# Optimization experiments

Measured on AMD Instinct MI355X. Metric: run time of the kernel, lower is better.

## Reference

```python
import jax, jax.numpy as jnp
import numpy as np

V, E, H, L = 32000, 1024, 1024, 2
B, T = 64, 256


def setup_inputs() -> dict:
    key = jax.random.key(0)
    ks = jax.random.split(key, 6)
    src = jax.random.randint(ks[0], (B, T), 0, V, dtype=jnp.int32)
    s_e = 1.0 / np.sqrt(H)
    emb = jax.random.normal(ks[1], (V, E), dtype=jnp.float32) * 0.02
    # stacked-layer LSTM params; layer 0 input = E == H so shapes are uniform
    W_ih = jax.random.uniform(ks[2], (L, 4 * H, H), dtype=jnp.float32, minval=-s_e, maxval=s_e)
    W_hh = jax.random.uniform(ks[3], (L, 4 * H, H), dtype=jnp.float32, minval=-s_e, maxval=s_e)
    b_ih = jax.random.uniform(ks[4], (L, 4 * H), dtype=jnp.float32, minval=-s_e, maxval=s_e)
    b_hh = jax.random.uniform(ks[5], (L, 4 * H), dtype=jnp.float32, minval=-s_e, maxval=s_e)
    return {"src": src, "emb": emb, "W_ih": W_ih, "W_hh": W_hh, "b_ih": b_ih, "b_hh": b_hh}


def _lstm_stack(embedded, W_ih, W_hh, b_ih, b_hh):
    # embedded: [B, T, E]
    Bsz = embedded.shape[0]
    h0 = jnp.zeros((L, Bsz, H), embedded.dtype)
    c0 = jnp.zeros((L, Bsz, H), embedded.dtype)

    def step(carry, x_t):
        h, c = carry  # each [L, B, H]
        x = x_t       # [B, E]
        new_h, new_c = [], []
        for l in range(L):
            gates = x @ W_ih[l].T + b_ih[l] + h[l] @ W_hh[l].T + b_hh[l]  # [B, 4H]
            i, f, g, o = jnp.split(gates, 4, axis=-1)
            c_t = jax.nn.sigmoid(f) * c[l] + jax.nn.sigmoid(i) * jnp.tanh(g)
            h_t = jax.nn.sigmoid(o) * jnp.tanh(c_t)
            new_h.append(h_t)
            new_c.append(c_t)
            x = h_t  # feed to next layer (dropout p=0)
        return (jnp.stack(new_h), jnp.stack(new_c)), x

    (h_n, c_n), outs = jax.lax.scan(step, (h0, c0), jnp.swapaxes(embedded, 0, 1))
    return jnp.swapaxes(outs, 0, 1), h_n, c_n  # [B,T,H], [L,B,H], [L,B,H]


def reference(src, emb, W_ih, W_hh, b_ih, b_hh):
    embedded = emb[src]  # [B, T, E]
    encoder_outputs, h_n, c_n = _lstm_stack(embedded, W_ih, W_hh, b_ih, b_hh)
    return encoder_outputs, (h_n, c_n)
```

## Files before the change

kernel.cpp:

```cpp
#include <hip/hip_runtime.h>
#include <hip/hip_bf16.h>

typedef __hip_bfloat16 bf16;
typedef __attribute__((ext_vector_type(8))) short s16x8;
typedef __attribute__((ext_vector_type(4))) float f32x4;
typedef __attribute__((ext_vector_type(4))) int   i32x4;

#define BATCH   64
#define SEQ     256
#define HID     1024
#define GATES   4096
#define NWG     256
#define THREADS 256
#define UNITS   8
#define NCOLS   32
#define ROWSTRIDE 2056
#define BH      (BATCH * HID)

#define HBASE_OFF  4096ull
#define WS_NEED    (HBASE_OFF + 2ull * SEQ * BH * 2)
#define H0_RS 8
#define H1_RS 2

#define OUT_HN  ((size_t)BATCH * SEQ * HID)
#define OUT_CN  (OUT_HN + 2ull * BATCH * HID)

__device__ __forceinline__ short f2bf(float f) {
    unsigned int u = __builtin_bit_cast(unsigned int, f);
    u = (u + 0x7fffu + ((u >> 16) & 1u)) >> 16;
    return (short)u;
}

#define GLD(i, OFF, CF) asm volatile("global_load_dwordx4 %0, %1, off offset:" OFF " " CF \
                                     : "=v"(h[i]) : "v"(xrow));
#define MM8(B0) \
    _Pragma("unroll") \
    for (int kk = (B0); kk < (B0) + 8; ++kk) { \
        s16x8 b0 = *(const s16x8*)(s0 + kk * 32); \
        s16x8 b1 = *(const s16x8*)(s1 + kk * 32); \
        s16x8 av = __builtin_bit_cast(s16x8, h[kk]); \
        a0 = __builtin_amdgcn_mfma_f32_16x16x32_bf16(av, b0, a0, 0, 0, 0); \
        a1 = __builtin_amdgcn_mfma_f32_16x16x32_bf16(av, b1, a1, 0, 0, 0); \
    }
#define GEMM_FN(NAME, CF) \
__device__ __forceinline__ void NAME(const bf16* xrow, const bf16* s0, const bf16* s1, \
                                     f32x4& a0, f32x4& a1) \
{ \
    i32x4 h[32]; \
    GLD(0,"0",CF)    GLD(1,"64",CF)   GLD(2,"128",CF)  GLD(3,"192",CF) \
    GLD(4,"256",CF)  GLD(5,"320",CF)  GLD(6,"384",CF)  GLD(7,"448",CF) \
    GLD(8,"512",CF)  GLD(9,"576",CF)  GLD(10,"640",CF) GLD(11,"704",CF) \
    GLD(12,"768",CF) GLD(13,"832",CF) GLD(14,"896",CF) GLD(15,"960",CF) \
    GLD(16,"1024",CF) GLD(17,"1088",CF) GLD(18,"1152",CF) GLD(19,"1216",CF) \
    GLD(20,"1280",CF) GLD(21,"1344",CF) GLD(22,"1408",CF) GLD(23,"1472",CF) \
    asm volatile("s_waitcnt vmcnt(16)"); __builtin_amdgcn_sched_barrier(0); \
    MM8(0) \
    GLD(24,"1536",CF) GLD(25,"1600",CF) GLD(26,"1664",CF) GLD(27,"1728",CF) \
    GLD(28,"1792",CF) GLD(29,"1856",CF) GLD(30,"1920",CF) GLD(31,"1984",CF) \
    asm volatile("s_waitcnt vmcnt(16)"); __builtin_amdgcn_sched_barrier(0); \
    MM8(8) \
    asm volatile("s_waitcnt vmcnt(8)");  __builtin_amdgcn_sched_barrier(0); \
    MM8(16) \
    asm volatile("s_waitcnt vmcnt(0)");  __builtin_amdgcn_sched_barrier(0); \
    MM8(24) \
}
GEMM_FN(gemm_bt, "sc0 sc1")
GEMM_FN(gemm_p,  "")

__device__ __forceinline__ void gemm_f32c(const float* xrow, const bf16* s0, const bf16* s1,
                                          f32x4& a0, f32x4& a1)
{
#pragma unroll
    for (int c = 0; c < 4; ++c) {
        f32x4 xv[16];
#pragma unroll
        for (int i = 0; i < 8; ++i) {
            const float* p = xrow + (c * 8 + i) * 32;
            xv[2 * i]     = *(const f32x4*)p;
            xv[2 * i + 1] = *(const f32x4*)(p + 4);
        }
#pragma unroll
        for (int i = 0; i < 8; ++i) {
            const int kk = c * 8 + i;
            s16x8 af;
#pragma unroll
            for (int j = 0; j < 4; ++j) {
                af[j]     = f2bf(xv[2 * i][j]);
                af[4 + j] = f2bf(xv[2 * i + 1][j]);
            }
            s16x8 b0 = *(const s16x8*)(s0 + kk * 32);
            s16x8 b1 = *(const s16x8*)(s1 + kk * 32);
            a0 = __builtin_amdgcn_mfma_f32_16x16x32_bf16(af, b0, a0, 0, 0, 0);
            a1 = __builtin_amdgcn_mfma_f32_16x16x32_bf16(af, b1, a1, 0, 0, 0);
        }
    }
}

__device__ __forceinline__ void wave_poll(unsigned int* f, int tgt, int* seen) {
    if (tgt <= 0 || *seen >= tgt) return;
    const int l = threadIdx.x & 63;
    unsigned int* p0 = f + l;
    unsigned int* p1 = f + 64 + l;
    int a, b;
    for (;;) {
        a = (int)__hip_atomic_load(p0, __ATOMIC_RELAXED, __HIP_MEMORY_SCOPE_AGENT);
        b = (int)__hip_atomic_load(p1, __ATOMIC_RELAXED, __HIP_MEMORY_SCOPE_AGENT);
        if (__all((a >= tgt) && (b >= tgt))) break;
        __builtin_amdgcn_s_sleep(1);
    }
    int v = (a < b) ? a : b;
#pragma unroll
    for (int off = 32; off; off >>= 1) {
        int w = __shfl_xor(v, off, 64);
        v = (w < v) ? w : v;
    }
    *seen = v;
    asm volatile("" ::: "memory");
}

__global__ void ws_init(unsigned int* p, int n) {
    for (int i = blockIdx.x * blockDim.x + threadIdx.x; i < n; i += gridDim.x * blockDim.x)
        p[i] = 0u;
}

__global__ void __launch_bounds__(THREADS, 1)
lstm_enc(const int* __restrict__ src, const float* __restrict__ Wemb,
         const float* __restrict__ Wih, const float* __restrict__ Whh,
         const float* __restrict__ bih, const float* __restrict__ bhh,
         float* __restrict__ out, bf16* __restrict__ hbuf, int hist_on)
{
    __shared__ __align__(16) bf16 slab[NCOLS][ROWSTRIDE];
    __shared__ float bias[NCOLS];

    const int wg    = blockIdx.x;
    const int layer = wg >> 7;
    const int wgl   = wg & 127;
    const int j0    = wgl * UNITS;
    const int tid   = threadIdx.x;
    const int lane  = tid & 63;
    const int wave  = tid >> 6;
    const int m     = lane & 15;
    const int q     = lane >> 4;
    const int kq    = q * 8;
    const int b_a   = wave * 16 + m;

    for (int r = 0; r < NCOLS; ++r) {
        int g = r >> 3, u = r & 7;
        size_t grow = (size_t)layer * GATES * HID + (size_t)(g * HID + j0 + u) * HID;
        int k = tid * 8;
        const float* s = (k < HID) ? (Wih + grow + k) : (Whh + grow + (k - HID));
        s16x8 v;
#pragma unroll
        for (int j = 0; j < 8; ++j) v[j] = f2bf(s[j]);
        *(s16x8*)&slab[r][k] = v;
    }
    if (tid < NCOLS) {
        int g = tid >> 3, u = tid & 7;
        int off = layer * GATES + g * HID + j0 + u;
        bias[tid] = bih[off] + bhh[off];
    }
    __syncthreads();

    unsigned int* flags = (unsigned int*)hbuf;
    bf16* hb = (bf16*)((char*)hbuf + HBASE_OFF);
    bf16* h0 = hb;
    bf16* h1 = hist_on ? hb + (size_t)SEQ * BH : hb + (size_t)H0_RS * BH;
    unsigned int* f0 = flags + wave * 128;
    unsigned int* f1 = flags + 512 + wave * 128;
    unsigned int* myflag = flags + layer * 512 + wave * 128 + wgl;

    const int u = m & 7;
    const float b_i = bias[u], b_f = bias[8 + u], b_g = bias[16 + u], b_o = bias[24 + u];
    float c_s[4] = {0.f, 0.f, 0.f, 0.f};
    int seenA = 0, seenB = 0;

    int sv = (layer == 0) ? src[b_a * SEQ] : 0;

    for (int t = 0; t < SEQ; ++t) {
        f32x4 acc0 = {0.f, 0.f, 0.f, 0.f};
        f32x4 acc1 = {0.f, 0.f, 0.f, 0.f};

        if (layer == 0) {
            const float* xF = Wemb + (size_t)sv * HID + kq;
            if (t + 1 < SEQ) sv = src[b_a * SEQ + t + 1];
            gemm_f32c(xF, &slab[m][kq], &slab[16 + m][kq], acc0, acc1);
            wave_poll(f0, t, &seenA);
            if (t >= 1) {
                if (hist_on)
                    gemm_p(h0 + (size_t)(t - 1) * BH + b_a * HID + kq,
                           &slab[m][HID + kq], &slab[16 + m][HID + kq], acc0, acc1);
                else
                    gemm_bt(h0 + (size_t)((t - 1) & (H0_RS - 1)) * BH + b_a * HID + kq,
                            &slab[m][HID + kq], &slab[16 + m][HID + kq], acc0, acc1);
            }
            if (!hist_on)
                wave_poll(f1, t - 7, &seenB);
        } else {
            wave_poll(f0, t + 1, &seenA);
            if (hist_on)
                gemm_p(h0 + (size_t)t * BH + b_a * HID + kq,
                       &slab[m][kq], &slab[16 + m][kq], acc0, acc1);
            else
                gemm_bt(h0 + (size_t)(t & (H0_RS - 1)) * BH + b_a * HID + kq,
                        &slab[m][kq], &slab[16 + m][kq], acc0, acc1);
            wave_poll(f1, t, &seenB);
            if (t >= 1) {
                if (hist_on)
                    gemm_p(h1 + (size_t)(t - 1) * BH + b_a * HID + kq,
                           &slab[m][HID + kq], &slab[16 + m][HID + kq], acc0, acc1);
                else
                    gemm_bt(h1 + (size_t)((t - 1) & (H1_RS - 1)) * BH + b_a * HID + kq,
                            &slab[m][HID + kq], &slab[16 + m][HID + kq], acc0, acc1);
            }
        }

        float hval[4];
#pragma unroll
        for (int r = 0; r < 4; ++r) {
            float p0 = __shfl_xor(acc0[r], 8, 64);
            float p1 = __shfl_xor(acc1[r], 8, 64);
            const bool lo = (m < 8);
            float gi = (lo ? acc0[r] : p0) + b_i;
            float gf = (lo ? p0 : acc0[r]) + b_f;
            float gg = (lo ? acc1[r] : p1) + b_g;
            float go = (lo ? p1 : acc1[r]) + b_o;
            float si = 1.f / (1.f + __expf(-gi));
            float sf = 1.f / (1.f + __expf(-gf));
            float so = 1.f / (1.f + __expf(-go));
            c_s[r] = sf * c_s[r] + si * tanhf(gg);
            hval[r] = so * tanhf(c_s[r]);
        }

        bf16* hw = (layer == 0)
            ? h0 + (size_t)(hist_on ? t : (t & (H0_RS - 1))) * BH
            : h1 + (size_t)(hist_on ? t : (t & (H1_RS - 1))) * BH;
        if (m < 8) {
#pragma unroll
            for (int r = 0; r < 4; ++r) {
                int R = wave * 16 + q * 4 + r;
                __hip_atomic_store((unsigned short*)(hw + (size_t)R * HID + j0 + u),
                                   (unsigned short)f2bf(hval[r]),
                                   __ATOMIC_RELAXED, __HIP_MEMORY_SCOPE_AGENT);
            }
        }
        asm volatile("s_waitcnt vmcnt(0)"); __builtin_amdgcn_sched_barrier(0);
        asm volatile("" ::: "memory");
        if (lane == 0)
            __hip_atomic_store(myflag, (unsigned int)(t + 1),
                               __ATOMIC_RELAXED, __HIP_MEMORY_SCOPE_AGENT);

        if (layer == 1 && m < 8) {
#pragma unroll
            for (int r = 0; r < 4; ++r) {
                int R = wave * 16 + q * 4 + r;
                out[((size_t)R * SEQ + t) * HID + j0 + u] = hval[r];
            }
        }
        if (t == SEQ - 1 && m < 8) {
#pragma unroll
            for (int r = 0; r < 4; ++r) {
                int R = wave * 16 + q * 4 + r;
                size_t o = ((size_t)layer * BATCH + R) * HID + j0 + u;
                out[OUT_HN + o] = hval[r];
                out[OUT_CN + o] = c_s[r];
            }
        }
    }
}

extern "C" void kernel_launch(void* const* d_in, const int* in_sizes, int n_in,
                              void* d_out, int out_size, void* d_ws, size_t ws_size,
                              hipStream_t stream) {
    const int*   src  = (const int*)d_in[0];
    const float* emb  = (const float*)d_in[1];
    const float* W_ih = (const float*)d_in[2];
    const float* W_hh = (const float*)d_in[3];
    const float* b_ih = (const float*)d_in[4];
    const float* b_hh = (const float*)d_in[5];
    float* out  = (float*)d_out;
    bf16*  hbuf = (bf16*)d_ws;

    ws_init<<<4, 256, 0, stream>>>((unsigned int*)d_ws, 1024);

    int hist_on = (ws_size >= (size_t)WS_NEED) ? 1 : 0;

    void* args[] = {&src, &emb, &W_ih, &W_hh, &b_ih, &b_hh, &out, &hbuf, &hist_on};
    hipLaunchCooperativeKernel((void*)lstm_enc, dim3(NWG), dim3(THREADS),
                               args, 0, stream);
}
```

Measured before the change: 3.552 ms.

## Overlap recurrent h-GEMM with per-chunk flag polling instead of full barrier

Replaces the whole-step wait on all producer workgroups with a fast check. If the check fails, the code polls flags per 128-column chunk group and starts loading and multiplying each chunk of h as soon as its producers are done, using a double-buffered register pipeline with a rotated start chunk per workgroup. This lets work on the recurrent matmul begin before the slowest producer finishes. The cost is more atomic polling traffic and more complex inline-asm wait counts. It only applies on the hist_on path.

```diff
diff --git a/kernel.cpp b/kernel.cpp
--- a/kernel.cpp
+++ b/kernel.cpp
@@ -118,6 +118,77 @@
     asm volatile("" ::: "memory");
 }
 
+__device__ __forceinline__ bool wave_probe(unsigned int* f, int tgt) {
+    const int l = threadIdx.x & 63;
+    int a = (int)__hip_atomic_load(f + l,      __ATOMIC_RELAXED, __HIP_MEMORY_SCOPE_AGENT);
+    int b = (int)__hip_atomic_load(f + 64 + l, __ATOMIC_RELAXED, __HIP_MEMORY_SCOPE_AGENT);
+    bool ok = __all((a >= tgt) && (b >= tgt));
+    asm volatile("" ::: "memory");
+    return ok;
+}
+
+__device__ __forceinline__ void gpoll(unsigned int* fch, int cg, int tgt) {
+    unsigned int* p = fch + cg * 16 + (threadIdx.x & 15);
+    for (;;) {
+        int v = (int)__hip_atomic_load(p, __ATOMIC_RELAXED, __HIP_MEMORY_SCOPE_AGENT);
+        if (__all(v >= tgt)) break;
+        __builtin_amdgcn_s_sleep(1);
+    }
+    asm volatile("" ::: "memory");
+}
+
+__device__ __forceinline__ void ld_chunk(const bf16* base, int cg, i32x4* hh) {
+    const bf16* p = base + cg * 128;
+    asm volatile("global_load_dwordx4 %0, %1, off"            : "=v"(hh[0]) : "v"(p));
+    asm volatile("global_load_dwordx4 %0, %1, off offset:64"  : "=v"(hh[1]) : "v"(p));
+    asm volatile("global_load_dwordx4 %0, %1, off offset:128" : "=v"(hh[2]) : "v"(p));
+    asm volatile("global_load_dwordx4 %0, %1, off offset:192" : "=v"(hh[3]) : "v"(p));
+}
+__device__ __forceinline__ void mm_chunk(const i32x4* hh, const bf16* s0, const bf16* s1,
+                                         int cg, f32x4& a0, f32x4& a1) {
+#pragma unroll
+    for (int j = 0; j < 4; ++j) {
+        const int kk = cg * 4 + j;
+        s16x8 b0 = *(const s16x8*)(s0 + kk * 32);
+        s16x8 b1 = *(const s16x8*)(s1 + kk * 32);
+        s16x8 av = __builtin_bit_cast(s16x8, hh[j]);
+        a0 = __builtin_amdgcn_mfma_f32_16x16x32_bf16(av, b0, a0, 0, 0, 0);
+        a1 = __builtin_amdgcn_mfma_f32_16x16x32_bf16(av, b1, a1, 0, 0, 0);
+    }
+}
+
+__device__ __forceinline__ void gemm_chunk(const bf16* xrow, const bf16* s0, const bf16* s1,
+                                           unsigned int* fch, int tgt, int grot,
+                                           f32x4& a0, f32x4& a1)
+{
+    if (wave_probe(fch, tgt)) {
+        gemm_p(xrow, s0, s1, a0, a1);
+        return;
+    }
+    i32x4 hA[4], hB[4];
+    {
+        const int c0 = grot & 7;
+        gpoll(fch, c0, tgt);
+        ld_chunk(xrow, c0, hA);
+    }
+#define STEP(i, CUR, NXT) \
+    { \
+        if ((i) < 7) { \
+            const int cn = (grot + (i) + 1) & 7; \
+            gpoll(fch, cn, tgt);                \
+            ld_chunk(xrow, cn, NXT); \
+            asm volatile("s_waitcnt vmcnt(4)"); \
+        } else { \
+            asm volatile("s_waitcnt vmcnt(0)"); \
+        } \
+        __builtin_amdgcn_sched_barrier(0); \
+        mm_chunk(CUR, s0, s1, (grot + (i)) & 7, a0, a1); \
+    }
+    STEP(0, hA, hB) STEP(1, hB, hA) STEP(2, hA, hB) STEP(3, hB, hA)
+    STEP(4, hA, hB) STEP(5, hB, hA) STEP(6, hA, hB) STEP(7, hB, hA)
+#undef STEP
+}
+
 __global__ void ws_init(unsigned int* p, int n) {
     for (int i = blockIdx.x * blockDim.x + threadIdx.x; i < n; i += gridDim.x * blockDim.x)
         p[i] = 0u;
@@ -143,6 +214,7 @@
     const int q     = lane >> 4;
     const int kq    = q * 8;
     const int b_a   = wave * 16 + m;
+    const int grot  = wgl >> 4;
 
     for (int r = 0; r < NCOLS; ++r) {
         int g = r >> 3, u = r & 7;
@@ -184,31 +256,33 @@
             const float* xF = Wemb + (size_t)sv * HID + kq;
             if (t + 1 < SEQ) sv = src[b_a * SEQ + t + 1];
             gemm_f32c(xF, &slab[m][kq], &slab[16 + m][kq], acc0, acc1);
-            wave_poll(f0, t, &seenA);
             if (t >= 1) {
                 if (hist_on)
-                    gemm_p(h0 + (size_t)(t - 1) * BH + b_a * HID + kq,
-                           &slab[m][HID + kq], &slab[16 + m][HID + kq], acc0, acc1);
-                else
+                    gemm_chunk(h0 + (size_t)(t - 1) * BH + b_a * HID + kq,
+                               &slab[m][HID + kq], &slab[16 + m][HID + kq],
+                               f0, t, grot, acc0, acc1);
+                else {
+                    wave_poll(f0, t, &seenA);
                     gemm_bt(h0 + (size_t)((t - 1) & (H0_RS - 1)) * BH + b_a * HID + kq,
                             &slab[m][HID + kq], &slab[16 + m][HID + kq], acc0, acc1);
+                }
             }
             if (!hist_on)
                 wave_poll(f1, t - 7, &seenB);
         } else {
             wave_poll(f0, t + 1, &seenA);
-            if (hist_on)
+            if (hist_on) {
                 gemm_p(h0 + (size_t)t * BH + b_a * HID + kq,
                        &slab[m][kq], &slab[16 + m][kq], acc0, acc1);
-            else
+                if (t >= 1)
+                    gemm_chunk(h1 + (size_t)(t - 1) * BH + b_a * HID + kq,
+                               &slab[m][HID + kq], &slab[16 + m][HID + kq],
+                               f1, t, grot, acc0, acc1);
+            } else {
                 gemm_bt(h0 + (size_t)(t & (H0_RS - 1)) * BH + b_a * HID + kq,
                         &slab[m][kq], &slab[16 + m][kq], acc0, acc1);
-            wave_poll(f1, t, &seenB);
-            if (t >= 1) {
-                if (hist_on)
-                    gemm_p(h1 + (size_t)(t - 1) * BH + b_a * HID + kq,
-                           &slab[m][HID + kq], &slab[16 + m][HID + kq], acc0, acc1);
-                else
+                wave_poll(f1, t, &seenB);
+                if (t >= 1)
                     gemm_bt(h1 + (size_t)((t - 1) & (H1_RS - 1)) * BH + b_a * HID + kq,
                             &slab[m][HID + kq], &slab[16 + m][HID + kq], acc0, acc1);
             }
```

Result: slower. 3.857 ms (+8.6%).
